# Performance work log

Hardware: AMD Instinct MI355X
Metric: run time of the kernel (lower is better)

Reference implementation:

```python
import jax, jax.numpy as jnp
import numpy as np

H = 16
EMB = 1024
DH = 64  # att_dim


def setup_inputs() -> dict:
    key = jax.random.key(0)
    k1, k2, k3 = jax.random.split(key, 3)
    B, T = 4, 2048
    x = jax.random.normal(k1, (B, T, EMB), dtype=jnp.float32)
    # torch nn.Linear weight layout: [out_features, in_features]
    w_qkv = jax.random.normal(k2, (3 * H * DH, EMB), dtype=jnp.float32) * (1.0 / np.sqrt(EMB))
    wo = jax.random.normal(k3, (EMB, H * DH), dtype=jnp.float32) * (1.0 / np.sqrt(H * DH))
    return {"x": x, "w_qkv": w_qkv, "wo": wo}


def reference(x, w_qkv, wo):
    B, T, C = x.shape
    qkv = jnp.einsum('btc,oc->bto', x, w_qkv)  # [B,T,3*H*DH]
    q, k, v = jnp.split(qkv, 3, axis=-1)
    # [B,H,T,DH]
    q = q.reshape(B, T, H, DH).transpose(0, 2, 1, 3)
    k = k.reshape(B, T, H, DH).transpose(0, 2, 1, 3)
    v = v.reshape(B, T, H, DH).transpose(0, 2, 1, 3)
    scale = 1.0 / np.sqrt(DH).astype(np.float32)
    scores = jnp.einsum('bhqd,bhkd->bhqk', q, k) * scale
    causal = jnp.tril(jnp.ones((T, T), dtype=bool))
    scores = jnp.where(causal, scores, jnp.finfo(scores.dtype).min)
    attn = jax.nn.softmax(scores, axis=-1)
    y = jnp.einsum('bhqk,bhkd->bhqd', attn, v)  # [B,H,T,DH]
    y = y.transpose(0, 2, 1, 3).reshape(B, T, H * DH)
    return jnp.einsum('bti,oi->bto', y, wo)
```

## Files before the change

kernel.cpp:

```cpp
#include <hip/hip_runtime.h>
#include <hip/hip_bf16.h>
#include <stdint.h>


typedef __attribute__((ext_vector_type(8))) short short8;
typedef __attribute__((ext_vector_type(4))) float floatx4;

extern "C" __device__ float __ocml_native_exp2_f32(float);

__device__ __forceinline__ ushort f2bf(float f) {
  uint32_t u = __float_as_uint(f);
  u += 0x7fff + ((u >> 16) & 1);
  return (ushort)(u >> 16);
}

#if __has_builtin(__builtin_amdgcn_cvt_pk_bf16_f32)
typedef __attribute__((ext_vector_type(2))) __bf16 bf16x2;
__device__ __forceinline__ uint32_t pack_bf16(float a, float b) {
  union { bf16x2 v; uint32_t u; } cv;
  cv.v = __builtin_amdgcn_cvt_pk_bf16_f32(a, b);
  return cv.u;
}
#else
__device__ __forceinline__ uint32_t pack_bf16(float a, float b) {
  uint32_t ua = __float_as_uint(a) + 0x8000u;
  uint32_t ub = __float_as_uint(b) + 0x8000u;
  return __builtin_amdgcn_perm(ub, ua, 0x07060302u);
}
#endif

__device__ __forceinline__ void gload16(const ushort* g, ushort* l) {
  __builtin_amdgcn_global_load_lds(
      (const __attribute__((address_space(1))) void*)g,
      (__attribute__((address_space(3))) void*)l, 16, 0, 0);
}

__global__ __launch_bounds__(256) void cvt3_kernel(const float* __restrict__ x,
                                                   const float* __restrict__ wq,
                                                   const float* __restrict__ wo,
                                                   ushort* __restrict__ xo,
                                                   ushort* __restrict__ wqo,
                                                   ushort* __restrict__ woo) {
  int i = blockIdx.x * 256 + threadIdx.x;
  const float* in; ushort* out; int idx;
  if (i < 2097152)      { in = x;  out = xo;  idx = i; }
  else if (i < 2883584) { in = wq; out = wqo; idx = i - 2097152; }
  else                  { in = wo; out = woo; idx = i - 2883584; }
  float4 v = ((const float4*)in)[idx];
  ushort4 o;
  o.x = f2bf(v.x); o.y = f2bf(v.y); o.z = f2bf(v.z); o.w = f2bf(v.w);
  ((ushort4*)out)[idx] = o;
}

__global__ __launch_bounds__(256, 2) void gemm256(const ushort* __restrict__ A,
                                                  const ushort* __restrict__ Bw,
                                                  ushort* __restrict__ qb,
                                                  ushort* __restrict__ kb,
                                                  ushort* __restrict__ vt) {
  constexpr int SLOT = 12288;
  __shared__ ushort ring[3 * SLOT];
  int tid = threadIdx.x;
  int lane = tid & 63, wave = tid >> 6;
  int lrow = lane & 15, quad = lane >> 4;
  int wm = wave >> 1, wn = wave & 1;
  int wm128 = wm * 128, wn64 = wn * 64;
  int m0 = blockIdx.x * 256, n0 = blockIdx.y * 128;

  int srow = tid >> 2;
  int schunk8 = ((tid & 3) ^ ((tid >> 3) & 3)) * 8;
  const ushort* Ag0 = A + (size_t)(m0 + srow) * 1024 + schunk8;
  const ushort* Bg0 = Bw + (size_t)(n0 + srow) * 1024 + schunk8;
  int fo2 = (quad ^ ((lrow >> 1) & 3)) * 8;

  const floatx4 zero4 = {0.f, 0.f, 0.f, 0.f};
  floatx4 acc[8][4];
#pragma unroll
  for (int i = 0; i < 8; i++)
#pragma unroll
    for (int j = 0; j < 4; j++) acc[i][j] = zero4;

  auto stage = [&](int t) {
    ushort* Sa = &ring[(t % 3) * SLOT];
    size_t kk = (size_t)t * 32;
    gload16(Ag0 + kk,                       &Sa[wave * 512]);
    gload16(Ag0 + kk + (size_t)64 * 1024,   &Sa[2048 + wave * 512]);
    gload16(Ag0 + kk + (size_t)128 * 1024,  &Sa[4096 + wave * 512]);
    gload16(Ag0 + kk + (size_t)192 * 1024,  &Sa[6144 + wave * 512]);
    gload16(Bg0 + kk,                       &Sa[8192 + wave * 512]);
    gload16(Bg0 + kk + (size_t)64 * 1024,   &Sa[10240 + wave * 512]);
  };

#define BARRIER(N_)                                                           \
  asm volatile("s_waitcnt vmcnt(" #N_ ")" ::: "memory");                      \
  __builtin_amdgcn_s_barrier();                                               \
  asm volatile("" ::: "memory");

#define COMPUTE(CUR_, DOSTAGE_, T_)                                           \
  {                                                                           \
    ushort* As_ = &ring[(CUR_)*SLOT];                                         \
    ushort* Bs_ = As_ + 8192;                                                 \
    short8 a_[8], b_[4];                                                      \
    _Pragma("unroll")                                                         \
    for (int mi = 0; mi < 8; mi++)                                            \
      a_[mi] = *(const short8*)(&As_[(wm128 + mi * 16 + lrow) * 32 + fo2]);   \
    _Pragma("unroll")                                                         \
    for (int nj = 0; nj < 4; nj++)                                            \
      b_[nj] = *(const short8*)(&Bs_[(wn64 + nj * 16 + lrow) * 32 + fo2]);    \
    if (DOSTAGE_) stage(T_);                                                  \
    __builtin_amdgcn_s_setprio(1);                                            \
    _Pragma("unroll")                                                         \
    for (int mi = 0; mi < 8; mi++)                                            \
      _Pragma("unroll")                                                       \
      for (int nj = 0; nj < 4; nj++)                                          \
        acc[mi][nj] = __builtin_amdgcn_mfma_f32_16x16x32_bf16(                \
            a_[mi], b_[nj], acc[mi][nj], 0, 0, 0);                            \
    __builtin_amdgcn_s_setprio(0);                                            \
  }

  stage(0); stage(1);
  int cur = 0;
#pragma unroll 1
  for (int u = 0; u < 30; ++u) {
    BARRIER(6)
    COMPUTE(cur, true, u + 2)
    cur = (cur == 2) ? 0 : cur + 1;
  }
  BARRIER(6)
  COMPUTE(cur, false, 0)
  cur = (cur == 2) ? 0 : cur + 1;
  BARRIER(0)
  COMPUTE(cur, false, 0)

#undef COMPUTE
#undef BARRIER

  ushort* sm = ring;
  int sec = n0 >> 10;
  int b_ = m0 >> 11, t0 = m0 & 2047;
  int hb = (n0 & 1023) >> 6;
  __syncthreads();

  if (sec < 2) {
    constexpr int CS = 136;
    float qs = (sec == 0) ? 0.18033688f : 1.0f;
    ushort* dst = (sec == 0) ? qb : kb;
#pragma unroll
    for (int mi = 0; mi < 8; mi++)
#pragma unroll
      for (int nj = 0; nj < 4; nj++)
#pragma unroll
        for (int r = 0; r < 4; r++)
          sm[(wm128 + mi * 16 + quad * 4 + r) * CS + wn64 + nj * 16 + lrow] =
              f2bf(acc[mi][nj][r] * qs);
    __syncthreads();
    int mrow = tid >> 3, kcol = tid & 7;
#pragma unroll
    for (int mi = 0; mi < 8; mi++)
#pragma unroll
      for (int hh = 0; hh < 2; hh++) {
        int mloc = mi * 32 + mrow;
        uint4 val = *(const uint4*)(&sm[mloc * CS + hh * 64 + kcol * 8]);
        int t = t0 + mloc, h = hb + hh;
        *(uint4*)(dst + ((size_t)(b_ * 16 + h) * 2048 + t) * 64 + kcol * 8) = val;
      }
  } else {
    constexpr int CS2 = 264;
#pragma unroll
    for (int mi = 0; mi < 8; mi++)
#pragma unroll
      for (int nj = 0; nj < 4; nj++) {
        uint2 w;
        w.x = pack_bf16(acc[mi][nj][0], acc[mi][nj][1]);
        w.y = pack_bf16(acc[mi][nj][2], acc[mi][nj][3]);
        *(uint2*)(&sm[(wn64 + nj * 16 + lrow) * CS2 + wm128 + mi * 16 +
                      quad * 4]) = w;
      }
    __syncthreads();
    int drow = tid >> 4, kcol = tid & 15;
#pragma unroll
    for (int di = 0; di < 8; di++)
#pragma unroll
      for (int mi2 = 0; mi2 < 2; mi2++) {
        int nloc = di * 16 + drow;
        int moff = mi2 * 128 + kcol * 8;
        uint4 val = *(const uint4*)(&sm[nloc * CS2 + moff]);
        int h = hb + (nloc >> 6), d = nloc & 63;
        *(uint4*)(vt + ((size_t)(b_ * 16 + h) * 64 + d) * 2048 + t0 + moff) =
            val;
      }
  }
}

__global__ __launch_bounds__(256) void gemm_out(const ushort* __restrict__ A,
                                                const ushort* __restrict__ Bw,
                                                float* __restrict__ Cf) {
  constexpr int SLOT = 8192;
  __shared__ ushort ring[3 * SLOT];
  int tid = threadIdx.x;
  int lane = tid & 63, wave = tid >> 6;
  int lrow = lane & 15, quad = lane >> 4;
  int wr = (wave >> 1) * 64, wc = (wave & 1) * 64;
  int m0 = blockIdx.x * 128, n0 = blockIdx.y * 128;

  int srow = tid >> 2;
  int schunk8 = ((tid & 3) ^ ((tid >> 3) & 3)) * 8;
  const ushort* Ag0 = A + (size_t)(m0 + srow) * 1024 + schunk8;
  const ushort* Ag1 = Ag0 + (size_t)64 * 1024;
  const ushort* Bg0 = Bw + (size_t)(n0 + srow) * 1024 + schunk8;
  const ushort* Bg1 = Bg0 + (size_t)64 * 1024;
  int fo2 = (quad ^ ((lrow >> 1) & 3)) * 8;

  const floatx4 zero4 = {0.f, 0.f, 0.f, 0.f};
  floatx4 acc[4][4];
#pragma unroll
  for (int i = 0; i < 4; i++)
#pragma unroll
    for (int j = 0; j < 4; j++) acc[i][j] = zero4;

  auto stage = [&](int t) {
    ushort* Sa = &ring[(t % 3) * SLOT];
    size_t kk = (size_t)t * 32;
    gload16(Ag0 + kk, &Sa[wave * 16 * 32]);
    gload16(Ag1 + kk, &Sa[(64 + wave * 16) * 32]);
    gload16(Bg0 + kk, &Sa[4096 + wave * 16 * 32]);
    gload16(Bg1 + kk, &Sa[4096 + (64 + wave * 16) * 32]);
  };

  short8 fAa[4], fAb[4], fBa[4], fBb[4];

#define READF(u_, FN)                                                         \
  {                                                                           \
    ushort* As_ = &ring[((u_) % 3) * SLOT];                                   \
    ushort* Bs_ = As_ + 4096;                                                 \
    _Pragma("unroll")                                                         \
    for (int mi = 0; mi < 4; mi++)                                            \
      FN##a[mi] = *(const short8*)(&As_[(wr + mi * 16 + lrow) * 32 + fo2]);   \
    _Pragma("unroll")                                                         \
    for (int nj = 0; nj < 4; nj++)                                            \
      FN##b[nj] = *(const short8*)(&Bs_[(wc + nj * 16 + lrow) * 32 + fo2]);   \
  }

#define MFMAS(FC)                                                             \
  {                                                                           \
    __builtin_amdgcn_s_setprio(1);                                            \
    _Pragma("unroll")                                                         \
    for (int mi = 0; mi < 4; mi++)                                            \
      _Pragma("unroll")                                                       \
      for (int nj = 0; nj < 4; nj++)                                          \
        acc[mi][nj] = __builtin_amdgcn_mfma_f32_16x16x32_bf16(                \
            FC##a[mi], FC##b[nj], acc[mi][nj], 0, 0, 0);                      \
    __builtin_amdgcn_s_setprio(0);                                            \
  }

#define BARRIER(N_)                                                           \
  asm volatile("s_waitcnt vmcnt(" #N_ ")" ::: "memory");                      \
  __builtin_amdgcn_s_barrier();                                               \
  asm volatile("" ::: "memory");

#define KITER(u_, N_, ISSUE_, FC, FN)                                         \
  {                                                                           \
    BARRIER(N_)                                                               \
    READF(u_, FN)                                                             \
    if (ISSUE_) stage((u_) + 2);                                              \
    MFMAS(FC)                                                                 \
  }

  stage(0); stage(1);
  BARRIER(4)
  READF(0, fA)
  stage(2);
#pragma unroll 1
  for (int p = 0; p < 14; ++p) {
    KITER(2 * p + 1, 4, true, fA, fB);
    KITER(2 * p + 2, 4, true, fB, fA);
  }
  KITER(29, 4, true, fA, fB);
  KITER(30, 4, false, fB, fA);
  KITER(31, 0, false, fA, fB);
  MFMAS(fB)

#undef KITER
#undef BARRIER
#undef MFMAS
#undef READF

#pragma unroll
  for (int mi = 0; mi < 4; mi++)
#pragma unroll
    for (int nj = 0; nj < 4; nj++)
#pragma unroll
      for (int r = 0; r < 4; r++) {
        int m = m0 + wr + mi * 16 + quad * 4 + r;
        int n = n0 + wc + nj * 16 + lrow;
        Cf[(size_t)m * 1024 + n] = acc[mi][nj][r];
      }
}

__global__ __launch_bounds__(512) void attn_kernel(const ushort* __restrict__ qg,
                                                   const ushort* __restrict__ kg,
                                                   const ushort* __restrict__ vg,
                                                   ushort* __restrict__ y) {
  __shared__ ushort Ks[64 * 64];
  __shared__ ushort Vs[64 * 64];
  __shared__ ushort Ps[8 * 16 * 72];
  int tid = threadIdx.x;
  int lane = tid & 63, wave = tid >> 6;
  int lrow = lane & 15, quad = lane >> 4;
  int gx = blockIdx.x, gy = blockIdx.y;
  int qt = 15 - (gy >> 3);
  int bh = (gy & 7) * 8 + gx;
  const ushort* qp = qg + (size_t)bh * 2048 * 64;
  const ushort* kp = kg + (size_t)bh * 2048 * 64;
  const ushort* vp = vg + (size_t)bh * 64 * 2048;
  int b = bh >> 4, h = bh & 15;
  int srow = tid >> 3, sc = tid & 7;
  int sswz = ((sc ^ (srow & 7)) * 8);
  int fo = (quad ^ (lrow & 7)) * 8;
  ushort* Pw = &Ps[wave * 16 * 72];

  const floatx4 zero4 = {0.f, 0.f, 0.f, 0.f};
  short8 ones;
#pragma unroll
  for (int i = 0; i < 8; i++) ones[i] = (short)0x3F80;

  int last = 2 * qt + 1;

  const ushort* qrow_p = qp + (size_t)((qt << 7) + wave * 16 + lrow) * 64;
  short8 a_q0 = *(const short8*)(qrow_p + quad * 8);
  short8 a_q1 = *(const short8*)(qrow_p + (quad ^ 4) * 8);

  uint4 kreg = *(const uint4*)(kp + (size_t)srow * 64 + sc * 8);
  uint4 vreg = *(const uint4*)(vp + (size_t)srow * 2048 + sc * 8);

  floatx4 l_acc = zero4;
  floatx4 o_acc[4];
#pragma unroll
  for (int j = 0; j < 4; j++) o_acc[j] = zero4;

#pragma unroll 1
  for (int kv = 0; kv <= last; kv++) {
    asm volatile("" ::: "memory");
    __builtin_amdgcn_s_barrier();
    asm volatile("" ::: "memory");
    *(uint4*)(&Ks[srow * 64 + sswz]) = kreg;
    *(uint4*)(&Vs[srow * 64 + sswz]) = vreg;
    if (kv < last) {
      kreg = *(const uint4*)(kp + (size_t)((kv + 1) * 64 + srow) * 64 + sc * 8);
      vreg = *(const uint4*)(vp + (size_t)srow * 2048 + (kv + 1) * 64 + sc * 8);
    }
    asm volatile("s_waitcnt lgkmcnt(0)" ::: "memory");
    __builtin_amdgcn_s_barrier();
    asm volatile("" ::: "memory");

    floatx4 s[4];
#pragma unroll
    for (int ct = 0; ct < 4; ct++) {
      short8 k0 = *(const short8*)(&Ks[(ct * 16 + lrow) * 64 + fo]);
      short8 k1 = *(const short8*)(&Ks[(ct * 16 + lrow) * 64 + (fo ^ 32)]);
      floatx4 z = zero4;
      z = __builtin_amdgcn_mfma_f32_16x16x32_bf16(k0, a_q0, z, 0, 0, 0);
      z = __builtin_amdgcn_mfma_f32_16x16x32_bf16(k1, a_q1, z, 0, 0, 0);
      s[ct] = z;
    }

    if (kv >= 2 * qt) {
      int qabs = (qt << 7) + wave * 16 + lrow;
      int kbase = (kv << 6) + quad * 4;
#pragma unroll
      for (int ct = 0; ct < 4; ct++)
#pragma unroll
        for (int r = 0; r < 4; r++)
          if (kbase + ct * 16 + r > qabs) s[ct][r] = -1e30f;
    }

#pragma unroll
    for (int ct = 0; ct < 4; ct++) {
      float p0 = __ocml_native_exp2_f32(s[ct][0]);
      float p1 = __ocml_native_exp2_f32(s[ct][1]);
      float p2 = __ocml_native_exp2_f32(s[ct][2]);
      float p3 = __ocml_native_exp2_f32(s[ct][3]);
      uint2 w;
      w.x = pack_bf16(p0, p1);
      w.y = pack_bf16(p2, p3);
      *(uint2*)(&Pw[lrow * 72 + ct * 16 + quad * 4]) = w;
    }
    asm volatile("" ::: "memory");

    short8 a_p0 = *(const short8*)(&Pw[lrow * 72 + quad * 8]);
    short8 a_p1 = *(const short8*)(&Pw[lrow * 72 + 32 + quad * 8]);
    l_acc = __builtin_amdgcn_mfma_f32_16x16x32_bf16(a_p0, ones, l_acc, 0, 0, 0);
    l_acc = __builtin_amdgcn_mfma_f32_16x16x32_bf16(a_p1, ones, l_acc, 0, 0, 0);
#pragma unroll
    for (int j = 0; j < 4; j++) {
      short8 v0 = *(const short8*)(&Vs[(j * 16 + lrow) * 64 + fo]);
      short8 v1 = *(const short8*)(&Vs[(j * 16 + lrow) * 64 + (fo ^ 32)]);
      o_acc[j] = __builtin_amdgcn_mfma_f32_16x16x32_bf16(a_p0, v0, o_acc[j], 0, 0, 0);
      o_acc[j] = __builtin_amdgcn_mfma_f32_16x16x32_bf16(a_p1, v1, o_acc[j], 0, 0, 0);
    }
  }

  float inv[4];
#pragma unroll
  for (int r = 0; r < 4; r++) inv[r] = 1.0f / l_acc[r];

#pragma unroll
  for (int j = 0; j < 4; j++)
#pragma unroll
    for (int r = 0; r < 4; r++) {
      int t = (qt << 7) + wave * 16 + quad * 4 + r;
      y[((size_t)b * 2048 + t) * 1024 + h * 64 + j * 16 + lrow] =
          f2bf(o_acc[j][r] * inv[r]);
    }
}

extern "C" void kernel_launch(void* const* d_in, const int* in_sizes, int n_in,
                              void* d_out, int out_size, void* d_ws, size_t ws_size,
                              hipStream_t stream) {
  const float* x     = (const float*)d_in[0];
  const float* w_qkv = (const float*)d_in[1];
  const float* wo    = (const float*)d_in[2];
  float* out = (float*)d_out;

  ushort* x_bf    = (ushort*)d_ws;
  ushort* wqkv_bf = x_bf + (size_t)8192 * 1024;
  ushort* wo_bf   = wqkv_bf + (size_t)3072 * 1024;
  ushort* qb      = wo_bf + (size_t)1024 * 1024;
  ushort* kb      = qb + (size_t)8388608;
  ushort* vt      = kb + (size_t)8388608;
  ushort* yb      = x_bf;

  cvt3_kernel<<<12288, 256, 0, stream>>>(x, w_qkv, wo, x_bf, wqkv_bf, wo_bf);
  gemm256<<<dim3(32, 24), 256, 0, stream>>>(x_bf, wqkv_bf, qb, kb, vt);
  attn_kernel<<<dim3(8, 128), 512, 0, stream>>>(qb, kb, vt, yb);
  gemm_out<<<dim3(64, 8), 256, 0, stream>>>(yb, wo_bf, out);
}
```

Measured before the change: 216.8 us.

## Process two 128-row query tiles per attention block to reuse K/V tiles

Each attention block now handles 256 query rows (two 16-row slices per wave) instead of 128, so every K/V tile staged in shared memory serves twice as many query rows and global K/V traffic and barriers per query drop. The first query slice skips the last two KV tiles, where it is fully masked. The grid is halved to 512 blocks with a new mapping of blocks to query tiles, and launch bounds ask for 4 waves per SIMD. The costs are higher register pressure, fewer blocks to balance the causal work, and a coarser tail.

```diff
diff --git a/kernel.cpp b/kernel.cpp
--- a/kernel.cpp
+++ b/kernel.cpp
@@ -296,19 +296,19 @@
       }
 }
 
-__global__ __launch_bounds__(512) void attn_kernel(const ushort* __restrict__ qg,
-                                                   const ushort* __restrict__ kg,
-                                                   const ushort* __restrict__ vg,
-                                                   ushort* __restrict__ y) {
+__global__ __launch_bounds__(512, 4) void attn_kernel(const ushort* __restrict__ qg,
+                                                      const ushort* __restrict__ kg,
+                                                      const ushort* __restrict__ vg,
+                                                      ushort* __restrict__ y) {
   __shared__ ushort Ks[64 * 64];
   __shared__ ushort Vs[64 * 64];
-  __shared__ ushort Ps[8 * 16 * 72];
+  __shared__ ushort Ps[8 * 32 * 72];
   int tid = threadIdx.x;
   int lane = tid & 63, wave = tid >> 6;
   int lrow = lane & 15, quad = lane >> 4;
-  int gx = blockIdx.x, gy = blockIdx.y;
-  int qt = 15 - (gy >> 3);
-  int bh = (gy & 7) * 8 + gx;
+  int gx = blockIdx.x, g = blockIdx.y;
+  int qt = (g < 32) ? (7 - (g >> 2)) : ((g - 32) >> 2);
+  int bh = ((g >= 32) ? 32 : 0) + (g & 3) * 8 + gx;
   const ushort* qp = qg + (size_t)bh * 2048 * 64;
   const ushort* kp = kg + (size_t)bh * 2048 * 64;
   const ushort* vp = vg + (size_t)bh * 64 * 2048;
@@ -316,29 +316,34 @@
   int srow = tid >> 3, sc = tid & 7;
   int sswz = ((sc ^ (srow & 7)) * 8);
   int fo = (quad ^ (lrow & 7)) * 8;
-  ushort* Pw = &Ps[wave * 16 * 72];
+  ushort* Pw = &Ps[wave * 32 * 72];
 
   const floatx4 zero4 = {0.f, 0.f, 0.f, 0.f};
   short8 ones;
 #pragma unroll
   for (int i = 0; i < 8; i++) ones[i] = (short)0x3F80;
 
-  int last = 2 * qt + 1;
-
-  const ushort* qrow_p = qp + (size_t)((qt << 7) + wave * 16 + lrow) * 64;
-  short8 a_q0 = *(const short8*)(qrow_p + quad * 8);
-  short8 a_q1 = *(const short8*)(qrow_p + (quad ^ 4) * 8);
+  int last = 4 * qt + 3;
+  int qbase = (qt << 8) + wave * 16 + lrow;
+
+  const ushort* qr0 = qp + (size_t)qbase * 64;
+  short8 a_q0 = *(const short8*)(qr0 + quad * 8);
+  short8 a_q1 = *(const short8*)(qr0 + (quad ^ 4) * 8);
+  const ushort* qr1 = qr0 + (size_t)128 * 64;
+  short8 a_q2 = *(const short8*)(qr1 + quad * 8);
+  short8 a_q3 = *(const short8*)(qr1 + (quad ^ 4) * 8);
 
   uint4 kreg = *(const uint4*)(kp + (size_t)srow * 64 + sc * 8);
   uint4 vreg = *(const uint4*)(vp + (size_t)srow * 2048 + sc * 8);
 
-  floatx4 l_acc = zero4;
-  floatx4 o_acc[4];
-#pragma unroll
-  for (int j = 0; j < 4; j++) o_acc[j] = zero4;
+  floatx4 l0 = zero4, l1 = zero4;
+  floatx4 o0[4], o1[4];
+#pragma unroll
+  for (int j = 0; j < 4; j++) { o0[j] = zero4; o1[j] = zero4; }
 
 #pragma unroll 1
   for (int kv = 0; kv <= last; kv++) {
+    bool do0 = (kv < 4 * qt + 2);
     asm volatile("" ::: "memory");
     __builtin_amdgcn_s_barrier();
     asm volatile("" ::: "memory");
@@ -352,64 +357,110 @@
     __builtin_amdgcn_s_barrier();
     asm volatile("" ::: "memory");
 
-    floatx4 s[4];
-#pragma unroll
-    for (int ct = 0; ct < 4; ct++) {
-      short8 k0 = *(const short8*)(&Ks[(ct * 16 + lrow) * 64 + fo]);
-      short8 k1 = *(const short8*)(&Ks[(ct * 16 + lrow) * 64 + (fo ^ 32)]);
-      floatx4 z = zero4;
-      z = __builtin_amdgcn_mfma_f32_16x16x32_bf16(k0, a_q0, z, 0, 0, 0);
-      z = __builtin_amdgcn_mfma_f32_16x16x32_bf16(k1, a_q1, z, 0, 0, 0);
-      s[ct] = z;
+    int kbase = (kv << 6) + quad * 4;
+
+    if (do0) {
+      floatx4 s[4];
+#pragma unroll
+      for (int ct = 0; ct < 4; ct++) {
+        short8 k0 = *(const short8*)(&Ks[(ct * 16 + lrow) * 64 + fo]);
+        short8 k1 = *(const short8*)(&Ks[(ct * 16 + lrow) * 64 + (fo ^ 32)]);
+        floatx4 z = zero4;
+        z = __builtin_amdgcn_mfma_f32_16x16x32_bf16(k0, a_q0, z, 0, 0, 0);
+        z = __builtin_amdgcn_mfma_f32_16x16x32_bf16(k1, a_q1, z, 0, 0, 0);
+        s[ct] = z;
+      }
+      if (kv >= 4 * qt) {
+#pragma unroll
+        for (int ct = 0; ct < 4; ct++)
+#pragma unroll
+          for (int r = 0; r < 4; r++)
+            if (kbase + ct * 16 + r > qbase) s[ct][r] = -1e30f;
+      }
+#pragma unroll
+      for (int ct = 0; ct < 4; ct++) {
+        uint2 w;
+        w.x = pack_bf16(__ocml_native_exp2_f32(s[ct][0]),
+                        __ocml_native_exp2_f32(s[ct][1]));
+        w.y = pack_bf16(__ocml_native_exp2_f32(s[ct][2]),
+                        __ocml_native_exp2_f32(s[ct][3]));
+        *(uint2*)(&Pw[lrow * 72 + ct * 16 + quad * 4]) = w;
+      }
     }
 
-    if (kv >= 2 * qt) {
-      int qabs = (qt << 7) + wave * 16 + lrow;
-      int kbase = (kv << 6) + quad * 4;
-#pragma unroll
-      for (int ct = 0; ct < 4; ct++)
-#pragma unroll
-        for (int r = 0; r < 4; r++)
-          if (kbase + ct * 16 + r > qabs) s[ct][r] = -1e30f;
-    }
-
-#pragma unroll
-    for (int ct = 0; ct < 4; ct++) {
-      float p0 = __ocml_native_exp2_f32(s[ct][0]);
-      float p1 = __ocml_native_exp2_f32(s[ct][1]);
-      float p2 = __ocml_native_exp2_f32(s[ct][2]);
-      float p3 = __ocml_native_exp2_f32(s[ct][3]);
-      uint2 w;
-      w.x = pack_bf16(p0, p1);
-      w.y = pack_bf16(p2, p3);
-      *(uint2*)(&Pw[lrow * 72 + ct * 16 + quad * 4]) = w;
+    {
+      floatx4 s[4];
+#pragma unroll
+      for (int ct = 0; ct < 4; ct++) {
+        short8 k0 = *(const short8*)(&Ks[(ct * 16 + lrow) * 64 + fo]);
+        short8 k1 = *(const short8*)(&Ks[(ct * 16 + lrow) * 64 + (fo ^ 32)]);
+        floatx4 z = zero4;
+        z = __builtin_amdgcn_mfma_f32_16x16x32_bf16(k0, a_q2, z, 0, 0, 0);
+        z = __builtin_amdgcn_mfma_f32_16x16x32_bf16(k1, a_q3, z, 0, 0, 0);
+        s[ct] = z;
+      }
+      if (kv >= 4 * qt + 2) {
+        int qabs1 = qbase + 128;
+#pragma unroll
+        for (int ct = 0; ct < 4; ct++)
+#pragma unroll
+          for (int r = 0; r < 4; r++)
+            if (kbase + ct * 16 + r > qabs1) s[ct][r] = -1e30f;
+      }
+#pragma unroll
+      for (int ct = 0; ct < 4; ct++) {
+        uint2 w;
+        w.x = pack_bf16(__ocml_native_exp2_f32(s[ct][0]),
+                        __ocml_native_exp2_f32(s[ct][1]));
+        w.y = pack_bf16(__ocml_native_exp2_f32(s[ct][2]),
+                        __ocml_native_exp2_f32(s[ct][3]));
+        *(uint2*)(&Pw[(16 + lrow) * 72 + ct * 16 + quad * 4]) = w;
+      }
     }
     asm volatile("" ::: "memory");
 
-    short8 a_p0 = *(const short8*)(&Pw[lrow * 72 + quad * 8]);
-    short8 a_p1 = *(const short8*)(&Pw[lrow * 72 + 32 + quad * 8]);
-    l_acc = __builtin_amdgcn_mfma_f32_16x16x32_bf16(a_p0, ones, l_acc, 0, 0, 0);
-    l_acc = __builtin_amdgcn_mfma_f32_16x16x32_bf16(a_p1, ones, l_acc, 0, 0, 0);
-#pragma unroll
-    for (int j = 0; j < 4; j++) {
-      short8 v0 = *(const short8*)(&Vs[(j * 16 + lrow) * 64 + fo]);
-      short8 v1 = *(const short8*)(&Vs[(j * 16 + lrow) * 64 + (fo ^ 32)]);
-      o_acc[j] = __builtin_amdgcn_mfma_f32_16x16x32_bf16(a_p0, v0, o_acc[j], 0, 0, 0);
-      o_acc[j] = __builtin_amdgcn_mfma_f32_16x16x32_bf16(a_p1, v1, o_acc[j], 0, 0, 0);
+    short8 ap10 = *(const short8*)(&Pw[(16 + lrow) * 72 + quad * 8]);
+    short8 ap11 = *(const short8*)(&Pw[(16 + lrow) * 72 + 32 + quad * 8]);
+    l1 = __builtin_amdgcn_mfma_f32_16x16x32_bf16(ap10, ones, l1, 0, 0, 0);
+    l1 = __builtin_amdgcn_mfma_f32_16x16x32_bf16(ap11, ones, l1, 0, 0, 0);
+    if (do0) {
+      short8 ap00 = *(const short8*)(&Pw[lrow * 72 + quad * 8]);
+      short8 ap01 = *(const short8*)(&Pw[lrow * 72 + 32 + quad * 8]);
+      l0 = __builtin_amdgcn_mfma_f32_16x16x32_bf16(ap00, ones, l0, 0, 0, 0);
+      l0 = __builtin_amdgcn_mfma_f32_16x16x32_bf16(ap01, ones, l0, 0, 0, 0);
+#pragma unroll
+      for (int j = 0; j < 4; j++) {
+        short8 v0 = *(const short8*)(&Vs[(j * 16 + lrow) * 64 + fo]);
+        short8 v1 = *(const short8*)(&Vs[(j * 16 + lrow) * 64 + (fo ^ 32)]);
+        o0[j] = __builtin_amdgcn_mfma_f32_16x16x32_bf16(ap00, v0, o0[j], 0, 0, 0);
+        o0[j] = __builtin_amdgcn_mfma_f32_16x16x32_bf16(ap01, v1, o0[j], 0, 0, 0);
+        o1[j] = __builtin_amdgcn_mfma_f32_16x16x32_bf16(ap10, v0, o1[j], 0, 0, 0);
+        o1[j] = __builtin_amdgcn_mfma_f32_16x16x32_bf16(ap11, v1, o1[j], 0, 0, 0);
+      }
+    } else {
+#pragma unroll
+      for (int j = 0; j < 4; j++) {
+        short8 v0 = *(const short8*)(&Vs[(j * 16 + lrow) * 64 + fo]);
+        short8 v1 = *(const short8*)(&Vs[(j * 16 + lrow) * 64 + (fo ^ 32)]);
+        o1[j] = __builtin_amdgcn_mfma_f32_16x16x32_bf16(ap10, v0, o1[j], 0, 0, 0);
+        o1[j] = __builtin_amdgcn_mfma_f32_16x16x32_bf16(ap11, v1, o1[j], 0, 0, 0);
+      }
     }
   }
 
-  float inv[4];
-#pragma unroll
-  for (int r = 0; r < 4; r++) inv[r] = 1.0f / l_acc[r];
+  float inv0[4], inv1[4];
+#pragma unroll
+  for (int r = 0; r < 4; r++) { inv0[r] = 1.0f / l0[r]; inv1[r] = 1.0f / l1[r]; }
 
 #pragma unroll
   for (int j = 0; j < 4; j++)
 #pragma unroll
     for (int r = 0; r < 4; r++) {
-      int t = (qt << 7) + wave * 16 + quad * 4 + r;
-      y[((size_t)b * 2048 + t) * 1024 + h * 64 + j * 16 + lrow] =
-          f2bf(o_acc[j][r] * inv[r]);
+      int t0 = (qt << 8) + wave * 16 + quad * 4 + r;
+      y[((size_t)b * 2048 + t0) * 1024 + h * 64 + j * 16 + lrow] =
+          f2bf(o0[j][r] * inv0[r]);
+      y[((size_t)b * 2048 + t0 + 128) * 1024 + h * 64 + j * 16 + lrow] =
+          f2bf(o1[j][r] * inv1[r]);
     }
 }
 
@@ -431,6 +482,6 @@
 
   cvt3_kernel<<<12288, 256, 0, stream>>>(x, w_qkv, wo, x_bf, wqkv_bf, wo_bf);
   gemm256<<<dim3(32, 24), 256, 0, stream>>>(x_bf, wqkv_bf, qb, kb, vt);
-  attn_kernel<<<dim3(8, 128), 512, 0, stream>>>(qb, kb, vt, yb);
+  attn_kernel<<<dim3(8, 64), 512, 0, stream>>>(qb, kb, vt, yb);
   gemm_out<<<dim3(64, 8), 256, 0, stream>>>(yb, wo_bf, out);
 }
```

Result: slower. 243.8 us (+12.5%).
